# Kernel optimization log

Hardware: AMD Instinct MI355X
Metric: run time of the kernel (lower is better)

## Reference

```python
import jax, jax.numpy as jnp
import numpy as np
from jax import lax

D_MODEL = 768
N_LAYER = 4
D_STATE = 16
D_CONV = 4
EXPAND = 2
VOCAB = 32000
B = 1
L = 1024
D_INNER = D_MODEL * EXPAND
EPS = 1e-5


def setup_inputs() -> dict:
    key = jax.random.key(0)
    ks = jax.random.split(key, 8)
    s = 0.02
    A_row = jnp.log(jnp.arange(1, D_STATE + 1, dtype=jnp.float32))  # log(1..N)
    return {
        "idx": jax.random.randint(ks[0], (B, L), 0, VOCAB),
        "embed": jax.random.normal(ks[1], (VOCAB, D_MODEL), jnp.float32) * s,
        "norm_w": jnp.ones((N_LAYER, D_MODEL), jnp.float32),
        "W_in": jax.random.normal(ks[2], (N_LAYER, 2 * D_INNER, D_MODEL), jnp.float32) * s,
        "conv_w": jax.random.normal(ks[3], (N_LAYER, D_INNER, 1, D_CONV), jnp.float32) * s,
        "conv_b": jnp.zeros((N_LAYER, D_INNER), jnp.float32),
        "W_x": jax.random.normal(ks[4], (N_LAYER, 2 * D_STATE + 1, D_INNER), jnp.float32) * s,
        "dt_w": jax.random.normal(ks[5], (N_LAYER, D_INNER, 1), jnp.float32) * s,
        "dt_b": jnp.zeros((N_LAYER, D_INNER), jnp.float32),
        "A_log": jnp.tile(A_row, (N_LAYER, D_INNER, 1)),
        "Dp": jnp.ones((N_LAYER, D_INNER), jnp.float32),
        "out_w": jax.random.normal(ks[6], (N_LAYER, D_MODEL, D_INNER), jnp.float32) * s,
        "norm_f_w": jnp.ones((D_MODEL,), jnp.float32),
    }


def rmsnorm(x, w):
    return x / jnp.sqrt(jnp.mean(x * x, axis=-1, keepdims=True) + EPS) * w


def selective_scan(xc, W_x, dt_w, dt_b, A_log, Dp):
    # xc: [B, L, D_INNER]
    A = -jnp.exp(A_log)                               # [D, N]
    xp = xc @ W_x.T                                   # [B, L, 2N+1]
    dt_r = xp[..., :1]
    Bv = xp[..., 1:1 + D_STATE]                       # [B, L, N]
    Cv = xp[..., 1 + D_STATE:]                        # [B, L, N]
    dt = jax.nn.softplus(dt_r * dt_w[:, 0] + dt_b)    # [B, L, D]
    dA = jnp.exp(dt[..., None] * A)                   # [B, L, D, N]
    dBx = dt[..., None] * Bv[:, :, None, :] * xc[..., None]  # [B, L, D, N]

    def step(h, inp):
        dA_t, dBx_t, C_t = inp
        h = dA_t * h + dBx_t                          # [B, D, N]
        y = jnp.einsum('bdn,bn->bd', h, C_t)          # [B, D]
        return h, y

    h0 = jnp.zeros((xc.shape[0], D_INNER, D_STATE), xc.dtype)
    _, ys = lax.scan(step, h0, (dA.transpose(1, 0, 2, 3),
                                dBx.transpose(1, 0, 2, 3),
                                Cv.transpose(1, 0, 2)))
    return ys.transpose(1, 0, 2) + xc * Dp            # [B, L, D]


def mamba_block(x, W_in, conv_w, conv_b, W_x, dt_w, dt_b, A_log, Dp, out_w):
    xz = x @ W_in.T                                   # [B, L, 2*D_INNER]
    x_ssm, z = jnp.split(xz, 2, axis=-1)
    # depthwise causal conv1d (torch pads both sides then keeps first L == left pad only)
    xc = lax.conv_general_dilated(x_ssm.transpose(0, 2, 1), conv_w, (1,),
                                  [(D_CONV - 1, 0)],
                                  feature_group_count=D_INNER,
                                  dimension_numbers=('NCH', 'OIH', 'NCH'))
    xc = (xc + conv_b[None, :, None]).transpose(0, 2, 1)
    xc = jax.nn.silu(xc)
    y = selective_scan(xc, W_x, dt_w, dt_b, A_log, Dp)
    y = y * jax.nn.silu(z)
    return y @ out_w.T


def reference(idx, embed, norm_w, W_in, conv_w, conv_b, W_x, dt_w, dt_b, A_log, Dp, out_w, norm_f_w):
    x = embed[idx]  # dropout in eval mode == identity
    for i in range(N_LAYER):
        x = x + mamba_block(rmsnorm(x, norm_w[i]), W_in[i], conv_w[i], conv_b[i],
                            W_x[i], dt_w[i], dt_b[i], A_log[i], Dp[i], out_w[i])
    x = rmsnorm(x, norm_f_w)
    logits = x @ embed.T  # tied lm_head
    return logits
```

## Files before the change

### kernel.cpp

```cpp
#include <hip/hip_runtime.h>

#define D_MODEL 768
#define D_INNER 1536
#define D_XZ    3072
#define D_STATE 16
#define LSEQ    1024
#define NCHUNK  32
#define CLEN    32

typedef float  floatx4 __attribute__((ext_vector_type(4)));
typedef __bf16 bf16x2  __attribute__((ext_vector_type(2)));
typedef __bf16 bf16x8  __attribute__((ext_vector_type(8)));

__device__ __forceinline__ float softplus_f(float x) {
  float e = __expf(-fabsf(x));
  return fmaxf(x, 0.f) + __logf(1.f + e);
}
__device__ __forceinline__ float silu_f(float x) {
  return x / (1.f + __expf(-x));
}
__device__ __forceinline__ void gload_lds16(const void* g, void* l) {
  __builtin_amdgcn_global_load_lds(
      (const __attribute__((address_space(1))) void*)g,
      (__attribute__((address_space(3))) void*)l, 16, 0, 0);
}

template <int N> __device__ __forceinline__ void waitcnt_vm() {
  asm volatile("s_waitcnt vmcnt(%0)" ::"n"(N) : "memory");
}
__device__ __forceinline__ void cfence() { asm volatile("" ::: "memory"); }

__global__ __launch_bounds__(256) void k_cvt(const float* __restrict__ src,
                                             __bf16* __restrict__ dst) {
  size_t i = ((size_t)blockIdx.x * 256 + threadIdx.x) * 8;
  float4 a = *(const float4*)(src + i);
  float4 b = *(const float4*)(src + i + 4);
  bf16x8 o;
  o[0] = (__bf16)a.x; o[1] = (__bf16)a.y; o[2] = (__bf16)a.z; o[3] = (__bf16)a.w;
  o[4] = (__bf16)b.x; o[5] = (__bf16)b.y; o[6] = (__bf16)b.z; o[7] = (__bf16)b.w;
  *(bf16x8*)(dst + i) = o;
}

__global__ __launch_bounds__(256) void k_gather(const float* __restrict__ embed,
                                                const int* __restrict__ idx,
                                                float* __restrict__ x) {
  int t = blockIdx.x;
  int tok = idx[t];
  const float* src = embed + (size_t)tok * D_MODEL;
  float* dst = x + (size_t)t * D_MODEL;
  for (int c = threadIdx.x; c < D_MODEL; c += 256) dst[c] = src[c];
}

__global__ __launch_bounds__(256) void k_rmsnorm_bf(const float* __restrict__ x,
                                                    const float* __restrict__ w,
                                                    __bf16* __restrict__ o) {
  int lane = threadIdx.x & 63;
  int row = blockIdx.x * 4 + (threadIdx.x >> 6);
  const float* xr = x + (size_t)row * D_MODEL;
  float2 v[6];
  float ss = 0.f;
#pragma unroll
  for (int i = 0; i < 6; i++) {
    v[i] = *(const float2*)(xr + lane * 2 + i * 128);
    ss += v[i].x * v[i].x + v[i].y * v[i].y;
  }
#pragma unroll
  for (int m = 32; m; m >>= 1) ss += __shfl_xor(ss, m, 64);
  float r = rsqrtf(ss * (1.f / 768.f) + 1e-5f);
  __bf16* orow = o + (size_t)row * D_MODEL;
#pragma unroll
  for (int i = 0; i < 6; i++) {
    float2 wv = *(const float2*)(w + lane * 2 + i * 128);
    bf16x2 p;
    p[0] = (__bf16)(v[i].x * r * wv.x);
    p[1] = (__bf16)(v[i].y * r * wv.y);
    *(bf16x2*)(orow + lane * 2 + i * 128) = p;
  }
}

template <int TM, int TN, int SK>
__global__ __launch_bounds__(256, 3) void k_gemm_bb(const __bf16* __restrict__ A,
                                                    const __bf16* __restrict__ B,
                                                    const float* res, float* __restrict__ C,
                                                    int M, int N, int K, int mTiles) {
  constexpr int MT  = TM / 32;
  constexpr int NTL = TN / 32;
  constexpr int NLA = TM / 64;
  constexpr int NLB = TN / 64;
  constexpr int NL  = NLA + NLB;
  __shared__ __attribute__((aligned(16))) __bf16 As[3][TM * 32];
  __shared__ __attribute__((aligned(16))) __bf16 Bs[3][TN * 32];
  const int tid = threadIdx.x;
  const int lane = tid & 63, wave = tid >> 6;
  const int fr = lane & 15, q = lane >> 4;

  int id = blockIdx.x;
  int per = gridDim.x >> 3;
  int v = (id & 7) * per + (id >> 3);
  int s = 0, rr = v;
  if (SK > 1) { int perS = gridDim.x / SK; s = v / perS; rr = v % perS; }
  int nt = rr / mTiles, mt_ = rr % mTiles;
  const int Mblk = mt_ * TM, Nblk = nt * TN;
  const int wm = (wave & 1) * (TM / 2), wn = (wave >> 1) * (TN / 2);
  const int Ks = K / SK;

  const int row_s = tid >> 2;
  const int cs = ((tid & 3) ^ ((row_s >> 1) & 3)) * 8;
  const __bf16* Ag = A + (size_t)(Mblk + row_s) * K + (size_t)s * Ks + cs;
  const __bf16* Bg = B + (size_t)(Nblk + row_s) * K + (size_t)s * Ks + cs;
  if (SK > 1) C += (size_t)s * M * N;

  floatx4 acc[MT][NTL];
#pragma unroll
  for (int i = 0; i < MT; i++)
#pragma unroll
    for (int j = 0; j < NTL; j++) {
      floatx4 z = {0.f, 0.f, 0.f, 0.f};
      acc[i][j] = z;
    }

  const int KT = Ks >> 5;

#define STAGE_T(t, b)                                                         \
  do {                                                                        \
    const int _k0 = (t) << 5;                                                 \
    _Pragma("unroll") for (int i = 0; i < NLA; i++)                           \
        gload_lds16(Ag + (size_t)(64 * i) * K + _k0,                          \
                    &As[b][tid * 8 + i * 2048]);                              \
    _Pragma("unroll") for (int i = 0; i < NLB; i++)                           \
        gload_lds16(Bg + (size_t)(64 * i) * K + _k0,                          \
                    &Bs[b][tid * 8 + i * 2048]);                              \
  } while (0)

#define STEP_T(b, WN)                                                         \
  do {                                                                        \
    waitcnt_vm<WN>();                                                         \
    __builtin_amdgcn_s_barrier();     \
    cfence();                                                                 \
    bf16x8 af[MT], bfr[NTL];                                                  \
    _Pragma("unroll") for (int mt = 0; mt < MT; mt++) {                       \
      const int R = wm + mt * 16 + fr;                                        \
      af[mt] = *(const bf16x8*)&As[b][R * 32 + ((q ^ ((R >> 1) & 3)) << 3)];  \
    }                                                                         \
    _Pragma("unroll") for (int ntl = 0; ntl < NTL; ntl++) {                   \
      const int R = wn + ntl * 16 + fr;                                       \
      bfr[ntl] = *(const bf16x8*)&Bs[b][R * 32 + ((q ^ ((R >> 1) & 3)) << 3)]; \
    }                                                                         \
    _Pragma("unroll") for (int mt = 0; mt < MT; mt++)                         \
      _Pragma("unroll") for (int ntl = 0; ntl < NTL; ntl++)                   \
        acc[mt][ntl] = __builtin_amdgcn_mfma_f32_16x16x32_bf16(               \
            af[mt], bfr[ntl], acc[mt][ntl], 0, 0, 0);                         \
    cfence();                                                                 \
    __builtin_amdgcn_s_barrier();              \
    cfence();                                                                 \
  } while (0)

  STAGE_T(0, 0);
  STAGE_T(1, 1);

  int bcur = 0, bpre = 2;
  for (int kt = 0; kt < KT - 2; ++kt) {
    STAGE_T(kt + 2, bpre);
    STEP_T(bcur, 2 * NL);
    bcur = (bcur == 2) ? 0 : bcur + 1;
    bpre = (bpre == 2) ? 0 : bpre + 1;
  }
  STEP_T(bcur, NL);
  bcur = (bcur == 2) ? 0 : bcur + 1;
  STEP_T(bcur, 0);

#undef STAGE_T
#undef STEP_T

#pragma unroll
  for (int mt = 0; mt < MT; mt++)
#pragma unroll
    for (int ntl = 0; ntl < NTL; ntl++) {
      int r = Mblk + wm + mt * 16 + q * 4;
      int c = Nblk + wn + ntl * 16 + fr;
#pragma unroll
      for (int i = 0; i < 4; i++) {
        size_t o = (size_t)(r + i) * N + c;
        float vv = acc[mt][ntl][i];
        if (res) vv += res[o];
        C[o] = vv;
      }
    }
}

__global__ __launch_bounds__(256) void k_redK(const float* __restrict__ p,
                                              float* __restrict__ x) {
  size_t i = ((size_t)blockIdx.x * 256 + threadIdx.x) * 4;
  float4 a  = *(float4*)(x + i);
  float4 p0 = *(const float4*)(p + i);
  float4 p1 = *(const float4*)(p + 786432 + i);
  float4 p2 = *(const float4*)(p + 2 * 786432 + i);
  float4 p3 = *(const float4*)(p + 3 * 786432 + i);
  a.x += ((p0.x + p1.x) + p2.x) + p3.x;
  a.y += ((p0.y + p1.y) + p2.y) + p3.y;
  a.z += ((p0.z + p1.z) + p2.z) + p3.z;
  a.w += ((p0.w + p1.w) + p2.w) + p3.w;
  *(float4*)(x + i) = a;
}

__global__ __launch_bounds__(256) void k_xpconv(const float* __restrict__ xz,
                                                const float* __restrict__ cw4,
                                                const float* __restrict__ cb,
                                                const float* __restrict__ Wx,
                                                float* __restrict__ xc,
                                                float* __restrict__ xp) {
  __shared__ float red[4][33];
  int t = blockIdx.x;
  int wave = threadIdx.x >> 6, lane = threadIdx.x & 63;
  float acc[33];
#pragma unroll
  for (int j = 0; j < 33; j++) acc[j] = 0.f;
  for (int ii = 0; ii < 6; ii++) {
    int k = wave * 384 + ii * 64 + lane;
    float4 w = *(const float4*)(cw4 + (size_t)k * 4);
    float wv[4] = {w.x, w.y, w.z, w.w};
    float vv = cb[k];
#pragma unroll
    for (int jj = 0; jj < 4; jj++) {
      int ts = t - 3 + jj;
      if (ts >= 0) vv += wv[jj] * xz[(size_t)ts * D_XZ + k];
    }
    float xcv = silu_f(vv);
    xc[(size_t)t * D_INNER + k] = xcv;
#pragma unroll
    for (int j = 0; j < 33; j++) acc[j] += xcv * Wx[(size_t)j * D_INNER + k];
  }
#pragma unroll
  for (int j = 0; j < 33; j++) {
    float s = acc[j];
#pragma unroll
    for (int m = 32; m; m >>= 1) s += __shfl_xor(s, m, 64);
    if (lane == j) red[wave][j] = s;
  }
  __syncthreads();
  int j = threadIdx.x;
  if (j < 33) xp[(size_t)t * 33 + j] = red[0][j] + red[1][j] + red[2][j] + red[3][j];
}

__global__ __launch_bounds__(256) void k_scan1(const float* __restrict__ xp,
                                               const float* __restrict__ xc,
                                               const float* __restrict__ dtw,
                                               const float* __restrict__ dtb,
                                               const float* __restrict__ Alog,
                                               float* __restrict__ hend,
                                               float* __restrict__ Pp) {
  __shared__ float sxp[CLEN * 33];
  int c = blockIdx.x;
  int d = blockIdx.y * 256 + threadIdx.x;
  for (int i = threadIdx.x; i < CLEN * 33; i += 256) sxp[i] = xp[(size_t)c * CLEN * 33 + i];
  __syncthreads();
  float Av[16];
#pragma unroll
  for (int n = 0; n < 16; n++) Av[n] = -__expf(Alog[(size_t)d * 16 + n]);
  float w_ = dtw[d], b_ = dtb[d];
  float h[16], P[16];
#pragma unroll
  for (int n = 0; n < 16; n++) { h[n] = 0.f; P[n] = 1.f; }
  const float* xcc = xc + (size_t)(c * CLEN) * D_INNER + d;
  for (int tl = 0; tl < CLEN; tl++) {
    float dtr = sxp[tl * 33];
    float xv = xcc[(size_t)tl * D_INNER];
    float dt = softplus_f(dtr * w_ + b_);
    float sx = dt * xv;
#pragma unroll
    for (int n = 0; n < 16; n++) {
      float dA = __expf(dt * Av[n]);
      h[n] = dA * h[n] + sx * sxp[tl * 33 + 1 + n];
      P[n] *= dA;
    }
  }
  size_t o = ((size_t)c * D_INNER + d) * 16;
#pragma unroll
  for (int n = 0; n < 16; n++) { hend[o + n] = h[n]; Pp[o + n] = P[n]; }
}

__global__ __launch_bounds__(256) void k_scan2(const float* __restrict__ xp,
                                               const float* __restrict__ xc,
                                               const float* __restrict__ xz,
                                               const float* __restrict__ dtw,
                                               const float* __restrict__ dtb,
                                               const float* __restrict__ Alog,
                                               const float* __restrict__ Dp,
                                               const float* __restrict__ hend,
                                               const float* __restrict__ Pp,
                                               __bf16* __restrict__ g) {
  __shared__ float sxp[CLEN * 33];
  int c = blockIdx.x;
  int d = blockIdx.y * 256 + threadIdx.x;
  for (int i = threadIdx.x; i < CLEN * 33; i += 256) sxp[i] = xp[(size_t)c * CLEN * 33 + i];
  __syncthreads();
  float Av[16];
#pragma unroll
  for (int n = 0; n < 16; n++) Av[n] = -__expf(Alog[(size_t)d * 16 + n]);
  float w_ = dtw[d], b_ = dtb[d], Dv = Dp[d];
  float h[16];
#pragma unroll
  for (int n = 0; n < 16; n++) h[n] = 0.f;
  for (int c2 = 0; c2 < c; c2++) {
    size_t o = ((size_t)c2 * D_INNER + d) * 16;
#pragma unroll
    for (int n4 = 0; n4 < 4; n4++) {
      float4 hv = *(const float4*)(hend + o + n4 * 4);
      float4 pv = *(const float4*)(Pp + o + n4 * 4);
      h[n4 * 4 + 0] = pv.x * h[n4 * 4 + 0] + hv.x;
      h[n4 * 4 + 1] = pv.y * h[n4 * 4 + 1] + hv.y;
      h[n4 * 4 + 2] = pv.z * h[n4 * 4 + 2] + hv.z;
      h[n4 * 4 + 3] = pv.w * h[n4 * 4 + 3] + hv.w;
    }
  }
  for (int tl = 0; tl < CLEN; tl++) {
    int t = c * CLEN + tl;
    float dtr = sxp[tl * 33];
    float xv = xc[(size_t)t * D_INNER + d];
    float dt = softplus_f(dtr * w_ + b_);
    float sx = dt * xv;
    float y = 0.f;
#pragma unroll
    for (int n = 0; n < 16; n++) {
      float dA = __expf(dt * Av[n]);
      h[n] = dA * h[n] + sx * sxp[tl * 33 + 1 + n];
      y += h[n] * sxp[tl * 33 + 17 + n];
    }
    float z = xz[(size_t)t * D_XZ + D_INNER + d];
    g[(size_t)t * D_INNER + d] = (__bf16)((y + xv * Dv) * silu_f(z));
  }
}

extern "C" void kernel_launch(void* const* d_in, const int* in_sizes, int n_in,
                              void* d_out, int out_size, void* d_ws, size_t ws_size,
                              hipStream_t stream) {
  const int*   idx     = (const int*)d_in[0];
  const float* embed   = (const float*)d_in[1];
  const float* norm_w  = (const float*)d_in[2];
  const float* W_in    = (const float*)d_in[3];
  const float* conv_w  = (const float*)d_in[4];
  const float* conv_b  = (const float*)d_in[5];
  const float* W_x     = (const float*)d_in[6];
  const float* dt_w    = (const float*)d_in[7];
  const float* dt_b    = (const float*)d_in[8];
  const float* A_log   = (const float*)d_in[9];
  const float* Dp      = (const float*)d_in[10];
  const float* out_w   = (const float*)d_in[11];
  const float* norm_fw = (const float*)d_in[12];
  float* out = (float*)d_out;

  float*  x    = (float*)d_ws;
  __bf16* xnb  = (__bf16*)(x + 786432);
  float*  xp   = (float*)(xnb + 786432);
  float*  Pp   = xp + 33792;
  __bf16* gbf  = (__bf16*)(Pp + 786432);
  __bf16* pool = gbf + 1572864;
  __bf16* W_in_bf  = pool;
  __bf16* out_w_bf = pool + 9437184;
  float*  xz   = (float*)(out_w_bf + 4718592);
  float*  xc   = xz + 3145728;
  float*  hend = xc + 1572864;
  __bf16* emb_bf = pool;

  k_cvt<<<4608, 256, 0, stream>>>(W_in, W_in_bf);
  k_cvt<<<2304, 256, 0, stream>>>(out_w, out_w_bf);

  k_gather<<<1024, 256, 0, stream>>>(embed, idx, x);

  for (int l = 0; l < 4; l++) {
    k_rmsnorm_bf<<<256, 256, 0, stream>>>(x, norm_w + (size_t)l * D_MODEL, xnb);
    k_gemm_bb<64, 64, 1><<<768, 256, 0, stream>>>(xnb, W_in_bf + (size_t)l * D_XZ * D_MODEL,
                                                  nullptr, xz, 1024, D_XZ, D_MODEL, 16);
    k_xpconv<<<1024, 256, 0, stream>>>(xz, conv_w + (size_t)l * D_INNER * 4,
                                       conv_b + (size_t)l * D_INNER,
                                       W_x + (size_t)l * 33 * D_INNER, xc, xp);
    k_scan1<<<dim3(NCHUNK, 6), 256, 0, stream>>>(xp, xc, dt_w + (size_t)l * D_INNER,
                                                 dt_b + (size_t)l * D_INNER,
                                                 A_log + (size_t)l * D_INNER * 16, hend, Pp);
    k_scan2<<<dim3(NCHUNK, 6), 256, 0, stream>>>(xp, xc, xz, dt_w + (size_t)l * D_INNER,
                                                 dt_b + (size_t)l * D_INNER,
                                                 A_log + (size_t)l * D_INNER * 16,
                                                 Dp + (size_t)l * D_INNER, hend, Pp, gbf);
    k_gemm_bb<64, 64, 4><<<768, 256, 0, stream>>>(gbf, out_w_bf + (size_t)l * D_MODEL * D_INNER,
                                                  nullptr, xz, 1024, D_MODEL, D_INNER, 16);
    k_redK<<<768, 256, 0, stream>>>(xz, x);
  }

  k_cvt<<<12000, 256, 0, stream>>>(embed, emb_bf);
  k_rmsnorm_bf<<<256, 256, 0, stream>>>(x, norm_fw, xnb);
  k_gemm_bb<128, 128, 1><<<2000, 256, 0, stream>>>(xnb, emb_bf, nullptr, out,
                                                   1024, 32000, D_MODEL, 8);
}
```

Before: 823.6 us.

## Fuse split-K reduction into rmsnorm, batch xpconv rows, stage scan inputs in LDS

The separate split-K reduction kernel is removed: the four partial out-projection sums are now added to the residual inside the next rmsnorm, which also writes the updated residual back. The conv/x-projection kernel now handles two timesteps per block, so each W_x load is reused twice. Both scan kernels stage the chunk's xc tile into shared memory with vector loads and read A_log as float4. Together these drop one launch per layer and some redundant global traffic, at the cost of more registers in xpconv and extra LDS in the scans.

```diff
diff --git a/kernel.cpp b/kernel.cpp
--- a/kernel.cpp
+++ b/kernel.cpp
@@ -52,6 +52,8 @@
 }
 
 __global__ __launch_bounds__(256) void k_rmsnorm_bf(const float* __restrict__ x,
+                                                    const float* __restrict__ p,
+                                                    float* __restrict__ xw,
                                                     const float* __restrict__ w,
                                                     __bf16* __restrict__ o) {
   int lane = threadIdx.x & 63;
@@ -61,7 +63,17 @@
   float ss = 0.f;
 #pragma unroll
   for (int i = 0; i < 6; i++) {
-    v[i] = *(const float2*)(xr + lane * 2 + i * 128);
+    int off = lane * 2 + i * 128;
+    v[i] = *(const float2*)(xr + off);
+    if (p) {
+      size_t e = (size_t)row * D_MODEL + off;
+      float2 p0 = *(const float2*)(p + e);
+      float2 p1 = *(const float2*)(p + 786432 + e);
+      float2 p2 = *(const float2*)(p + 2 * 786432 + e);
+      float2 p3 = *(const float2*)(p + 3 * 786432 + e);
+      v[i].x += ((p0.x + p1.x) + p2.x) + p3.x;
+      v[i].y += ((p0.y + p1.y) + p2.y) + p3.y;
+    }
     ss += v[i].x * v[i].x + v[i].y * v[i].y;
   }
 #pragma unroll
@@ -70,11 +82,13 @@
   __bf16* orow = o + (size_t)row * D_MODEL;
 #pragma unroll
   for (int i = 0; i < 6; i++) {
-    float2 wv = *(const float2*)(w + lane * 2 + i * 128);
-    bf16x2 p;
-    p[0] = (__bf16)(v[i].x * r * wv.x);
-    p[1] = (__bf16)(v[i].y * r * wv.y);
-    *(bf16x2*)(orow + lane * 2 + i * 128) = p;
+    int off = lane * 2 + i * 128;
+    if (p) *(float2*)(xw + (size_t)row * D_MODEL + off) = v[i];
+    float2 wv = *(const float2*)(w + off);
+    bf16x2 pk;
+    pk[0] = (__bf16)(v[i].x * r * wv.x);
+    pk[1] = (__bf16)(v[i].y * r * wv.y);
+    *(bf16x2*)(orow + off) = pk;
   }
 }
 
@@ -135,7 +149,7 @@
 #define STEP_T(b, WN)                                                         \
   do {                                                                        \
     waitcnt_vm<WN>();                                                         \
-    __builtin_amdgcn_s_barrier();     \
+    __builtin_amdgcn_s_barrier();                                             \
     cfence();                                                                 \
     bf16x8 af[MT], bfr[NTL];                                                  \
     _Pragma("unroll") for (int mt = 0; mt < MT; mt++) {                       \
@@ -151,7 +165,7 @@
         acc[mt][ntl] = __builtin_amdgcn_mfma_f32_16x16x32_bf16(               \
             af[mt], bfr[ntl], acc[mt][ntl], 0, 0, 0);                         \
     cfence();                                                                 \
-    __builtin_amdgcn_s_barrier();              \
+    __builtin_amdgcn_s_barrier();                                             \
     cfence();                                                                 \
   } while (0)
 
@@ -188,58 +202,60 @@
     }
 }
 
-__global__ __launch_bounds__(256) void k_redK(const float* __restrict__ p,
-                                              float* __restrict__ x) {
-  size_t i = ((size_t)blockIdx.x * 256 + threadIdx.x) * 4;
-  float4 a  = *(float4*)(x + i);
-  float4 p0 = *(const float4*)(p + i);
-  float4 p1 = *(const float4*)(p + 786432 + i);
-  float4 p2 = *(const float4*)(p + 2 * 786432 + i);
-  float4 p3 = *(const float4*)(p + 3 * 786432 + i);
-  a.x += ((p0.x + p1.x) + p2.x) + p3.x;
-  a.y += ((p0.y + p1.y) + p2.y) + p3.y;
-  a.z += ((p0.z + p1.z) + p2.z) + p3.z;
-  a.w += ((p0.w + p1.w) + p2.w) + p3.w;
-  *(float4*)(x + i) = a;
-}
-
-__global__ __launch_bounds__(256) void k_xpconv(const float* __restrict__ xz,
-                                                const float* __restrict__ cw4,
-                                                const float* __restrict__ cb,
-                                                const float* __restrict__ Wx,
-                                                float* __restrict__ xc,
-                                                float* __restrict__ xp) {
-  __shared__ float red[4][33];
-  int t = blockIdx.x;
+__global__ __launch_bounds__(256, 2) void k_xpconv(const float* __restrict__ xz,
+                                                   const float* __restrict__ cw4,
+                                                   const float* __restrict__ cb,
+                                                   const float* __restrict__ Wx,
+                                                   float* __restrict__ xc,
+                                                   float* __restrict__ xp) {
+  __shared__ float red[2][4][33];
+  int t0 = blockIdx.x * 2;
   int wave = threadIdx.x >> 6, lane = threadIdx.x & 63;
-  float acc[33];
-#pragma unroll
-  for (int j = 0; j < 33; j++) acc[j] = 0.f;
+  float acc0[33], acc1[33];
+#pragma unroll
+  for (int j = 0; j < 33; j++) { acc0[j] = 0.f; acc1[j] = 0.f; }
   for (int ii = 0; ii < 6; ii++) {
     int k = wave * 384 + ii * 64 + lane;
     float4 w = *(const float4*)(cw4 + (size_t)k * 4);
     float wv[4] = {w.x, w.y, w.z, w.w};
-    float vv = cb[k];
+    float cbk = cb[k];
+    float vv0 = cbk, vv1 = cbk;
 #pragma unroll
     for (int jj = 0; jj < 4; jj++) {
-      int ts = t - 3 + jj;
-      if (ts >= 0) vv += wv[jj] * xz[(size_t)ts * D_XZ + k];
-    }
-    float xcv = silu_f(vv);
-    xc[(size_t)t * D_INNER + k] = xcv;
-#pragma unroll
-    for (int j = 0; j < 33; j++) acc[j] += xcv * Wx[(size_t)j * D_INNER + k];
+      int ts = t0 - 3 + jj;
+      if (ts >= 0) vv0 += wv[jj] * xz[(size_t)ts * D_XZ + k];
+    }
+#pragma unroll
+    for (int jj = 0; jj < 4; jj++) {
+      int ts = t0 - 2 + jj;
+      if (ts >= 0) vv1 += wv[jj] * xz[(size_t)ts * D_XZ + k];
+    }
+    float xc0 = silu_f(vv0);
+    float xc1 = silu_f(vv1);
+    xc[(size_t)t0 * D_INNER + k] = xc0;
+    xc[(size_t)(t0 + 1) * D_INNER + k] = xc1;
+#pragma unroll
+    for (int j = 0; j < 33; j++) {
+      float wx = Wx[(size_t)j * D_INNER + k];
+      acc0[j] += xc0 * wx;
+      acc1[j] += xc1 * wx;
+    }
   }
 #pragma unroll
   for (int j = 0; j < 33; j++) {
-    float s = acc[j];
-#pragma unroll
-    for (int m = 32; m; m >>= 1) s += __shfl_xor(s, m, 64);
-    if (lane == j) red[wave][j] = s;
+    float s0 = acc0[j], s1 = acc1[j];
+#pragma unroll
+    for (int m = 32; m; m >>= 1) {
+      s0 += __shfl_xor(s0, m, 64);
+      s1 += __shfl_xor(s1, m, 64);
+    }
+    if (lane == j) { red[0][wave][j] = s0; red[1][wave][j] = s1; }
   }
   __syncthreads();
-  int j = threadIdx.x;
-  if (j < 33) xp[(size_t)t * 33 + j] = red[0][j] + red[1][j] + red[2][j] + red[3][j];
+  int wv2 = threadIdx.x >> 6, jl = threadIdx.x & 63;
+  if (wv2 < 2 && jl < 33)
+    xp[(size_t)(t0 + wv2) * 33 + jl] =
+        red[wv2][0][jl] + red[wv2][1][jl] + red[wv2][2][jl] + red[wv2][3][jl];
 }
 
 __global__ __launch_bounds__(256) void k_scan1(const float* __restrict__ xp,
@@ -250,21 +266,35 @@
                                                float* __restrict__ hend,
                                                float* __restrict__ Pp) {
   __shared__ float sxp[CLEN * 33];
+  __shared__ float sxc[CLEN * 256];
   int c = blockIdx.x;
-  int d = blockIdx.y * 256 + threadIdx.x;
+  int dblk = blockIdx.y * 256;
+  int d = dblk + threadIdx.x;
   for (int i = threadIdx.x; i < CLEN * 33; i += 256) sxp[i] = xp[(size_t)c * CLEN * 33 + i];
+  {
+    const float* src = xc + (size_t)(c * CLEN) * D_INNER + dblk;
+    for (int i = threadIdx.x; i < CLEN * 64; i += 256) {
+      int row = i >> 6, c4 = i & 63;
+      *(float4*)&sxc[row * 256 + c4 * 4] = *(const float4*)(src + (size_t)row * D_INNER + c4 * 4);
+    }
+  }
   __syncthreads();
   float Av[16];
-#pragma unroll
-  for (int n = 0; n < 16; n++) Av[n] = -__expf(Alog[(size_t)d * 16 + n]);
+  {
+    const float4* Ar = (const float4*)(Alog + (size_t)d * 16);
+    float4 a0 = Ar[0], a1 = Ar[1], a2 = Ar[2], a3 = Ar[3];
+    Av[0] = -__expf(a0.x); Av[1] = -__expf(a0.y); Av[2] = -__expf(a0.z); Av[3] = -__expf(a0.w);
+    Av[4] = -__expf(a1.x); Av[5] = -__expf(a1.y); Av[6] = -__expf(a1.z); Av[7] = -__expf(a1.w);
+    Av[8] = -__expf(a2.x); Av[9] = -__expf(a2.y); Av[10] = -__expf(a2.z); Av[11] = -__expf(a2.w);
+    Av[12] = -__expf(a3.x); Av[13] = -__expf(a3.y); Av[14] = -__expf(a3.z); Av[15] = -__expf(a3.w);
+  }
   float w_ = dtw[d], b_ = dtb[d];
   float h[16], P[16];
 #pragma unroll
   for (int n = 0; n < 16; n++) { h[n] = 0.f; P[n] = 1.f; }
-  const float* xcc = xc + (size_t)(c * CLEN) * D_INNER + d;
   for (int tl = 0; tl < CLEN; tl++) {
     float dtr = sxp[tl * 33];
-    float xv = xcc[(size_t)tl * D_INNER];
+    float xv = sxc[tl * 256 + threadIdx.x];
     float dt = softplus_f(dtr * w_ + b_);
     float sx = dt * xv;
 #pragma unroll
@@ -290,13 +320,28 @@
                                                const float* __restrict__ Pp,
                                                __bf16* __restrict__ g) {
   __shared__ float sxp[CLEN * 33];
+  __shared__ float sxc[CLEN * 256];
   int c = blockIdx.x;
-  int d = blockIdx.y * 256 + threadIdx.x;
+  int dblk = blockIdx.y * 256;
+  int d = dblk + threadIdx.x;
   for (int i = threadIdx.x; i < CLEN * 33; i += 256) sxp[i] = xp[(size_t)c * CLEN * 33 + i];
+  {
+    const float* src = xc + (size_t)(c * CLEN) * D_INNER + dblk;
+    for (int i = threadIdx.x; i < CLEN * 64; i += 256) {
+      int row = i >> 6, c4 = i & 63;
+      *(float4*)&sxc[row * 256 + c4 * 4] = *(const float4*)(src + (size_t)row * D_INNER + c4 * 4);
+    }
+  }
   __syncthreads();
   float Av[16];
-#pragma unroll
-  for (int n = 0; n < 16; n++) Av[n] = -__expf(Alog[(size_t)d * 16 + n]);
+  {
+    const float4* Ar = (const float4*)(Alog + (size_t)d * 16);
+    float4 a0 = Ar[0], a1 = Ar[1], a2 = Ar[2], a3 = Ar[3];
+    Av[0] = -__expf(a0.x); Av[1] = -__expf(a0.y); Av[2] = -__expf(a0.z); Av[3] = -__expf(a0.w);
+    Av[4] = -__expf(a1.x); Av[5] = -__expf(a1.y); Av[6] = -__expf(a1.z); Av[7] = -__expf(a1.w);
+    Av[8] = -__expf(a2.x); Av[9] = -__expf(a2.y); Av[10] = -__expf(a2.z); Av[11] = -__expf(a2.w);
+    Av[12] = -__expf(a3.x); Av[13] = -__expf(a3.y); Av[14] = -__expf(a3.z); Av[15] = -__expf(a3.w);
+  }
   float w_ = dtw[d], b_ = dtb[d], Dv = Dp[d];
   float h[16];
 #pragma unroll
@@ -315,8 +360,9 @@
   }
   for (int tl = 0; tl < CLEN; tl++) {
     int t = c * CLEN + tl;
+    float z = xz[(size_t)t * D_XZ + D_INNER + d];
     float dtr = sxp[tl * 33];
-    float xv = xc[(size_t)t * D_INNER + d];
+    float xv = sxc[tl * 256 + threadIdx.x];
     float dt = softplus_f(dtr * w_ + b_);
     float sx = dt * xv;
     float y = 0.f;
@@ -326,7 +372,6 @@
       h[n] = dA * h[n] + sx * sxp[tl * 33 + 1 + n];
       y += h[n] * sxp[tl * 33 + 17 + n];
     }
-    float z = xz[(size_t)t * D_XZ + D_INNER + d];
     g[(size_t)t * D_INNER + d] = (__bf16)((y + xv * Dv) * silu_f(z));
   }
 }
@@ -368,12 +413,13 @@
   k_gather<<<1024, 256, 0, stream>>>(embed, idx, x);
 
   for (int l = 0; l < 4; l++) {
-    k_rmsnorm_bf<<<256, 256, 0, stream>>>(x, norm_w + (size_t)l * D_MODEL, xnb);
+    k_rmsnorm_bf<<<256, 256, 0, stream>>>(x, l ? xz : nullptr, x,
+                                          norm_w + (size_t)l * D_MODEL, xnb);
     k_gemm_bb<64, 64, 1><<<768, 256, 0, stream>>>(xnb, W_in_bf + (size_t)l * D_XZ * D_MODEL,
                                                   nullptr, xz, 1024, D_XZ, D_MODEL, 16);
-    k_xpconv<<<1024, 256, 0, stream>>>(xz, conv_w + (size_t)l * D_INNER * 4,
-                                       conv_b + (size_t)l * D_INNER,
-                                       W_x + (size_t)l * 33 * D_INNER, xc, xp);
+    k_xpconv<<<512, 256, 0, stream>>>(xz, conv_w + (size_t)l * D_INNER * 4,
+                                      conv_b + (size_t)l * D_INNER,
+                                      W_x + (size_t)l * 33 * D_INNER, xc, xp);
     k_scan1<<<dim3(NCHUNK, 6), 256, 0, stream>>>(xp, xc, dt_w + (size_t)l * D_INNER,
                                                  dt_b + (size_t)l * D_INNER,
                                                  A_log + (size_t)l * D_INNER * 16, hend, Pp);
@@ -383,11 +429,10 @@
                                                  Dp + (size_t)l * D_INNER, hend, Pp, gbf);
     k_gemm_bb<64, 64, 4><<<768, 256, 0, stream>>>(gbf, out_w_bf + (size_t)l * D_MODEL * D_INNER,
                                                   nullptr, xz, 1024, D_MODEL, D_INNER, 16);
-    k_redK<<<768, 256, 0, stream>>>(xz, x);
-  }
-
+  }
+
+  k_rmsnorm_bf<<<256, 256, 0, stream>>>(x, xz, x, norm_fw, xnb);
   k_cvt<<<12000, 256, 0, stream>>>(embed, emb_bf);
-  k_rmsnorm_bf<<<256, 256, 0, stream>>>(x, norm_fw, xnb);
   k_gemm_bb<128, 128, 1><<<2000, 256, 0, stream>>>(xnb, emb_bf, nullptr, out,
                                                    1024, 32000, D_MODEL, 8);
 }
```

Result: no change. 838.7 us (+1.8%).
